# Optimization experiments

Hardware: AMD Instinct MI355X
Metric: run time of the kernel (lower is better)

The kernel has to match this reference:

```python
import jax, jax.numpy as jnp
import numpy as np

D_MODEL = 256
D_ENC_M = 256  # mel encoder dim (keys/values), sets temperature = sqrt(D_ENC_M)
D_ENC_T = 256  # text encoder dim (queries)
LN_EPS = 1e-5


def setup_inputs() -> dict:
    key = jax.random.key(0)
    ks = jax.random.split(key, 9)
    B, MEL_LEN, SRC_LEN = 16, 2048, 512
    mel_encoding = jax.random.normal(ks[0], (B, MEL_LEN, D_ENC_M), dtype=jnp.float32)
    text_encoding = jax.random.normal(ks[1], (B, SRC_LEN, D_ENC_T), dtype=jnp.float32)
    mel_mask = jax.random.randint(ks[2], (B, MEL_LEN), 0, 2).astype(bool)
    src_mask = jax.random.randint(ks[3], (B, SRC_LEN), 0, 2).astype(bool)
    # Linear weights (no bias), xavier-uniform style scale
    def xavier(k, shape):
        fan_in, fan_out = shape[1], shape[0]
        lim = jnp.sqrt(6.0 / (fan_in + fan_out))
        return jax.random.uniform(k, shape, jnp.float32, -lim, lim)
    Wq = xavier(ks[4], (D_MODEL, D_ENC_T))
    Wk = xavier(ks[5], (D_MODEL, D_ENC_M))
    Wv = xavier(ks[6], (D_MODEL, D_ENC_M))
    gamma = jnp.ones((D_MODEL,), jnp.float32)
    beta = jnp.zeros((D_MODEL,), jnp.float32)
    return {"mel_encoding": mel_encoding, "text_encoding": text_encoding,
            "mel_mask": mel_mask, "src_mask": src_mask,
            "Wq": Wq, "Wk": Wk, "Wv": Wv, "gamma": gamma, "beta": beta}


def reference(mel_encoding, text_encoding, mel_mask, src_mask, Wq, Wk, Wv, gamma, beta):
    # QKV projections (nn.Linear, bias=False): y = x @ W^T
    q = jnp.einsum('btd,md->btm', text_encoding, Wq)   # [B, src_len, d_model]
    k = jnp.einsum('bsd,md->bsm', mel_encoding, Wk)    # [B, mel_len, d_model]
    v = jnp.einsum('bsd,md->bsm', mel_encoding, Wv)    # [B, mel_len, d_model]
    temperature = jnp.asarray(D_ENC_M, jnp.float32) ** 0.5
    attn = jnp.einsum('btm,bsm->bts', q, k) / temperature  # [B, src_len, mel_len]
    # pre-softmax fill over mel (key) padding
    attn = jnp.where(mel_mask[:, None, :], -jnp.inf, attn)
    attn = jax.nn.softmax(attn, axis=2)
    # post-softmax zeroing over src (query) padding
    attn = jnp.where(src_mask[:, :, None], 0.0, attn)
    output = jnp.einsum('bts,bsm->btm', attn, v)  # [B, src_len, d_model]
    # dropout is identity in eval mode; LayerNorm over last dim
    mu = jnp.mean(output, axis=-1, keepdims=True)
    var = jnp.mean(jnp.square(output - mu), axis=-1, keepdims=True)
    output = (output - mu) * jax.lax.rsqrt(var + LN_EPS) * gamma + beta
    return (output, attn)
```

## Files before the change

### kernel.cpp

```cpp
#include <hip/hip_runtime.h>
#include <hip/hip_bf16.h>
#include <stdint.h>

#define DMODEL 256
#define BATCH  16
#define MEL    2048
#define SRC    512

typedef __attribute__((ext_vector_type(8))) short bf16x8;
typedef __attribute__((ext_vector_type(4))) short short4v;
typedef __attribute__((ext_vector_type(4))) float f32x4;

__device__ inline short f2bf(float f) {
    union { float f; uint32_t u; } c{f};
    uint32_t u = c.u;
    u += 0x7FFFu + ((u >> 16) & 1u);
    return (short)(u >> 16);
}

__device__ inline bf16x8 cvt8(const float* p) {
    const f32x4* q = reinterpret_cast<const f32x4*>(p);
    f32x4 a = q[0], b = q[1];
    bf16x8 r;
    r[0] = f2bf(a[0]); r[1] = f2bf(a[1]); r[2] = f2bf(a[2]); r[3] = f2bf(a[3]);
    r[4] = f2bf(b[0]); r[5] = f2bf(b[1]); r[6] = f2bf(b[2]); r[7] = f2bf(b[3]);
    return r;
}

__global__ __launch_bounds__(256)
void proj_all_kernel(const float* __restrict__ mel, const float* __restrict__ text,
                     const float* __restrict__ Wq, const float* __restrict__ Wk,
                     const float* __restrict__ Wv,
                     short* __restrict__ qbf, short* __restrict__ kbf,
                     short* __restrict__ vt) {
    __shared__ char SMEM[36864];
    short* As = (short*)SMEM;
    short* Bs = (short*)SMEM + 128 * 72;

    const int tid = threadIdx.x;
    const int lane = tid & 63, w = tid >> 6;
    const int lr = lane & 15, lk = lane >> 4;
    const int wr = w >> 1, wc = w & 1;

    const int u = blockIdx.x;
    const int xcd = u & 7, slot = u >> 3;

    const float *Af, *Bf; short* C; int ldc;
    size_t aro, bro, coff;
    if (slot < 128) {
        const int g = slot >> 2, m = slot & 3;
        const int st = 32 * xcd + g;
        const int b = st >> 4;
        const size_t mr0 = (size_t)(st & 15) * 128;
        if (m < 2) {
            aro = (size_t)b * MEL + mr0;
            bro = (size_t)m * 128;
            Af = mel; Bf = Wk; C = kbf; ldc = DMODEL;
            coff = aro * DMODEL + bro;
        } else {
            aro = (size_t)(m - 2) * 128;
            bro = (size_t)b * MEL + mr0;
            Af = Wv; Bf = mel; C = vt + (size_t)b * DMODEL * MEL; ldc = MEL;
            coff = aro * MEL + mr0;
        }
    } else {
        const int qi = 16 * xcd + (slot - 128);
        aro = (size_t)(qi >> 1) * 128;
        bro = (size_t)(qi & 1) * 128;
        Af = text; Bf = Wq; C = qbf; ldc = DMODEL;
        coff = aro * DMODEL + bro;
    }
    C += coff;

    bf16x8 sA[4], sB[4];
    auto STAGE = [&](int kt) {
#pragma unroll
        for (int i = 0; i < 4; ++i) {
            int idx = i * 256 + tid;
            int row = idx >> 3, c8 = (idx & 7) * 8;
            sA[i] = cvt8(Af + (aro + row) * 256 + kt * 64 + c8);
            sB[i] = cvt8(Bf + (bro + row) * 256 + kt * 64 + c8);
        }
    };

    STAGE(0);
    f32x4 acc[4][4];
#pragma unroll
    for (int m = 0; m < 4; ++m)
#pragma unroll
        for (int n = 0; n < 4; ++n) acc[m][n] = (f32x4){0.f, 0.f, 0.f, 0.f};

    for (int kt = 0; kt < 4; ++kt) {
        __syncthreads();
#pragma unroll
        for (int i = 0; i < 4; ++i) {
            int idx = i * 256 + tid;
            int row = idx >> 3, c8 = (idx & 7) * 8;
            *(bf16x8*)&As[row * 72 + c8] = sA[i];
            *(bf16x8*)&Bs[row * 72 + c8] = sB[i];
        }
        __syncthreads();
        if (kt < 3) STAGE(kt + 1);
#pragma unroll
        for (int kt2 = 0; kt2 < 2; ++kt2) {
            bf16x8 af[4], bfr[4];
#pragma unroll
            for (int m = 0; m < 4; ++m)
                af[m] = *(const bf16x8*)&As[(64 * wr + 16 * m + lr) * 72 + kt2 * 32 + 8 * lk];
#pragma unroll
            for (int n = 0; n < 4; ++n)
                bfr[n] = *(const bf16x8*)&Bs[(64 * wc + 16 * n + lr) * 72 + kt2 * 32 + 8 * lk];
#pragma unroll
            for (int m = 0; m < 4; ++m)
#pragma unroll
                for (int n = 0; n < 4; ++n)
                    acc[m][n] = __builtin_amdgcn_mfma_f32_16x16x32_bf16(af[m], bfr[n], acc[m][n], 0, 0, 0);
        }
    }

    __syncthreads();
    short* Cs = (short*)SMEM;
#pragma unroll
    for (int m = 0; m < 4; ++m)
#pragma unroll
        for (int n = 0; n < 4; ++n)
#pragma unroll
            for (int r = 0; r < 4; ++r)
                Cs[(64 * wr + 16 * m + 4 * lk + r) * 136 + 64 * wc + 16 * n + lr] =
                    f2bf(acc[m][n][r]);
    __syncthreads();
#pragma unroll
    for (int i = 0; i < 8; ++i) {
        int idx = i * 256 + tid;
        int row = idx >> 4, c8 = (idx & 15) * 8;
        *(bf16x8*)&C[(size_t)row * ldc + c8] = *(const bf16x8*)&Cs[row * 136 + c8];
    }
}

__global__ __launch_bounds__(256)
void sgemm_kernel(const short* __restrict__ qbf, const short* __restrict__ kbf,
                  const int* __restrict__ mel_mask,
                  float* __restrict__ attn,
                  float* __restrict__ pmax, float* __restrict__ psum) {
    __shared__ char SMEM[36864];
    short* As = (short*)SMEM;
    short* Bs = (short*)SMEM + 128 * 72;

    const int tid = threadIdx.x;
    const int lane = tid & 63, w = tid >> 6;
    const int lr = lane & 15, lk = lane >> 4;
    const int wr = w >> 1, wc = w & 1;

    const int bid = blockIdx.x;
    const int xcd = bid & 7, j = bid >> 3;
    const int z = 2 * xcd + (j >> 6);
    const int t = j & 63;
    const int x = t & 3, y = t >> 2;

    const short* A = qbf + (size_t)z * SRC * DMODEL + (size_t)x * 128 * DMODEL;
    const short* B = kbf + (size_t)z * MEL * DMODEL + (size_t)y * 128 * DMODEL;
    float* Cw = attn + (size_t)z * SRC * MEL + (size_t)x * 128 * MEL + (size_t)y * 128;

    bf16x8 sA[4], sB[4];
    auto STAGE = [&](int kt) {
#pragma unroll
        for (int i = 0; i < 4; ++i) {
            int idx = i * 256 + tid;
            int row = idx >> 3, c8 = (idx & 7) * 8;
            sA[i] = *(const bf16x8*)(A + (size_t)row * DMODEL + kt * 64 + c8);
            sB[i] = *(const bf16x8*)(B + (size_t)row * DMODEL + kt * 64 + c8);
        }
    };

    STAGE(0);
    f32x4 acc[4][4];
#pragma unroll
    for (int m = 0; m < 4; ++m)
#pragma unroll
        for (int n = 0; n < 4; ++n) acc[m][n] = (f32x4){0.f, 0.f, 0.f, 0.f};

    for (int kt = 0; kt < 4; ++kt) {
        __syncthreads();
#pragma unroll
        for (int i = 0; i < 4; ++i) {
            int idx = i * 256 + tid;
            int row = idx >> 3, c8 = (idx & 7) * 8;
            *(bf16x8*)&As[row * 72 + c8] = sA[i];
            *(bf16x8*)&Bs[row * 72 + c8] = sB[i];
        }
        __syncthreads();
        if (kt < 3) STAGE(kt + 1);
#pragma unroll
        for (int kt2 = 0; kt2 < 2; ++kt2) {
            bf16x8 af[4], bfr[4];
#pragma unroll
            for (int m = 0; m < 4; ++m)
                af[m] = *(const bf16x8*)&As[(64 * wr + 16 * m + lr) * 72 + kt2 * 32 + 8 * lk];
#pragma unroll
            for (int n = 0; n < 4; ++n)
                bfr[n] = *(const bf16x8*)&Bs[(64 * wc + 16 * n + lr) * 72 + kt2 * 32 + 8 * lk];
#pragma unroll
            for (int m = 0; m < 4; ++m)
#pragma unroll
                for (int n = 0; n < 4; ++n)
                    acc[m][n] = __builtin_amdgcn_mfma_f32_16x16x32_bf16(af[m], bfr[n], acc[m][n], 0, 0, 0);
        }
    }

    bool msk[4];
#pragma unroll
    for (int n = 0; n < 4; ++n)
        msk[n] = mel_mask[z * MEL + y * 128 + 64 * wc + 16 * n + lr] != 0;

    __syncthreads();
    float* Cs = (float*)SMEM;
#pragma unroll
    for (int half = 0; half < 2; ++half) {
        if (wr == half) {
#pragma unroll
            for (int m = 0; m < 4; ++m)
#pragma unroll
                for (int n = 0; n < 4; ++n)
#pragma unroll
                    for (int r = 0; r < 4; ++r)
                        Cs[(16 * m + 4 * lk + r) * 132 + 64 * wc + 16 * n + lr] =
                            msk[n] ? -1e30f : acc[m][n][r] * 0.0625f;
        }
        __syncthreads();
#pragma unroll
        for (int i = 0; i < 8; ++i) {
            int idx = i * 256 + tid;
            int row = idx >> 5, c4 = (idx & 31) * 4;
            *(f32x4*)&Cw[(size_t)(half * 64 + row) * MEL + c4] = *(const f32x4*)&Cs[row * 132 + c4];
        }
        {
            const int rrow = tid >> 2, seg = tid & 3;
            const f32x4* crow = (const f32x4*)(Cs + rrow * 132 + seg * 32);
            float m8 = -3.0e38f;
#pragma unroll
            for (int jj = 0; jj < 8; ++jj) {
                f32x4 v = crow[jj];
#pragma unroll
                for (int e = 0; e < 4; ++e) m8 = fmaxf(m8, v[e]);
            }
            m8 = fmaxf(m8, __shfl_xor(m8, 1));
            m8 = fmaxf(m8, __shfl_xor(m8, 2));
            float s8 = 0.f;
#pragma unroll
            for (int jj = 0; jj < 8; ++jj) {
                f32x4 v = crow[jj];
#pragma unroll
                for (int e = 0; e < 4; ++e) s8 += __expf(v[e] - m8);
            }
            s8 += __shfl_xor(s8, 1);
            s8 += __shfl_xor(s8, 2);
            if (seg == 0) {
                int grow = z * SRC + x * 128 + half * 64 + rrow;
                pmax[y * 8192 + grow] = m8;
                psum[y * 8192 + grow] = s8;
            }
        }
        __syncthreads();
    }
}

__global__ __launch_bounds__(512)
void rowred_kernel(const float* __restrict__ pmax, const float* __restrict__ psum,
                   const int* __restrict__ src_mask,
                   float* __restrict__ Mrow, float* __restrict__ Minv) {
    const int row = blockIdx.x * 512 + threadIdx.x;
    float M = -3.0e38f;
#pragma unroll
    for (int i = 0; i < 16; ++i) M = fmaxf(M, pmax[i * 8192 + row]);
    float Z = 0.f;
#pragma unroll
    for (int i = 0; i < 16; ++i)
        Z += psum[i * 8192 + row] * __expf(pmax[i * 8192 + row] - M);
    Mrow[row] = M;
    Minv[row] = (src_mask[row] || !(Z > 0.f)) ? 0.f : 1.f / Z;
}

__global__ __launch_bounds__(512)
void pv_ln_kernel(float* __restrict__ attn, const short* __restrict__ vt,
                  const float* __restrict__ gamma, const float* __restrict__ beta,
                  const float* __restrict__ Mrow, const float* __restrict__ Minv,
                  float* __restrict__ out) {
    __shared__ char SMEM[42496];
    short* As = (short*)SMEM;
    short* Bs = (short*)(SMEM + 4608);
    float* red = (float*)(SMEM + 41472);
    float* Ost = (float*)(SMEM + 4608);

    const int tid = threadIdx.x;
    const int lane = tid & 63, w = tid >> 6;
    const int lr = lane & 15, lk = lane >> 4;
    const int wr = w >> 2, wc = w & 3;

    const int bid = blockIdx.x;
    const int xcd = bid & 7, j = bid >> 3;
    const int b = 2 * xcd + (j >> 4);
    const int mt = j & 15;
    const size_t row0 = (size_t)mt * 32;

    float* A = attn + (size_t)b * SRC * MEL + row0 * MEL;
    const short* Bv = vt + (size_t)b * DMODEL * MEL;

    float gm[4], bt[4];
#pragma unroll
    for (int n = 0; n < 4; ++n) {
        gm[n] = gamma[64 * wc + 16 * n + lr];
        bt[n] = beta[64 * wc + 16 * n + lr];
    }

    const int a_row = tid >> 4, a_c4 = (tid & 15) * 4;
    const float Mr = Mrow[(size_t)b * SRC + row0 + a_row];
    const float Iv = Minv[(size_t)b * SRC + row0 + a_row];

    f32x4 sAv; bf16x8 sB[4];
    auto STAGE = [&](int kt) {
        sAv = *(const f32x4*)(A + (size_t)a_row * MEL + kt * 64 + a_c4);
#pragma unroll
        for (int i = 0; i < 4; ++i) {
            int idx = i * 512 + tid;
            int row = idx >> 3, c8 = (idx & 7) * 8;
            sB[i] = *(const bf16x8*)(Bv + (size_t)row * MEL + kt * 64 + c8);
        }
    };

    STAGE(0);
    f32x4 acc[4];
#pragma unroll
    for (int n = 0; n < 4; ++n) acc[n] = (f32x4){0.f, 0.f, 0.f, 0.f};

    for (int kt = 0; kt < MEL / 64; ++kt) {
        __syncthreads();
        {
            f32x4 p;
#pragma unroll
            for (int e = 0; e < 4; ++e) p[e] = __expf(sAv[e] - Mr) * Iv;
            *(f32x4*)(A + (size_t)a_row * MEL + kt * 64 + a_c4) = p;
            short4v a4 = { f2bf(p[0]), f2bf(p[1]), f2bf(p[2]), f2bf(p[3]) };
            *(short4v*)&As[a_row * 72 + a_c4] = a4;
#pragma unroll
            for (int i = 0; i < 4; ++i) {
                int idx = i * 512 + tid;
                int row = idx >> 3, c8 = (idx & 7) * 8;
                *(bf16x8*)&Bs[row * 72 + c8] = sB[i];
            }
        }
        __syncthreads();
        if (kt + 1 < MEL / 64) STAGE(kt + 1);
#pragma unroll
        for (int kt2 = 0; kt2 < 2; ++kt2) {
            bf16x8 af = *(const bf16x8*)&As[(16 * wr + lr) * 72 + kt2 * 32 + 8 * lk];
#pragma unroll
            for (int n = 0; n < 4; ++n) {
                bf16x8 bfr = *(const bf16x8*)&Bs[(64 * wc + 16 * n + lr) * 72 + kt2 * 32 + 8 * lk];
                acc[n] = __builtin_amdgcn_mfma_f32_16x16x32_bf16(af, bfr, acc[n], 0, 0, 0);
            }
        }
    }

    float s1[4] = {0.f, 0.f, 0.f, 0.f}, s2[4] = {0.f, 0.f, 0.f, 0.f};
#pragma unroll
    for (int n = 0; n < 4; ++n)
#pragma unroll
        for (int r = 0; r < 4; ++r) {
            s1[r] += acc[n][r];
            s2[r] += acc[n][r] * acc[n][r];
        }
#pragma unroll
    for (int off = 8; off; off >>= 1)
#pragma unroll
        for (int r = 0; r < 4; ++r) {
            s1[r] += __shfl_xor(s1[r], off);
            s2[r] += __shfl_xor(s2[r], off);
        }
    __syncthreads();
    if (lr == 0) {
#pragma unroll
        for (int r = 0; r < 4; ++r) {
            red[(16 * wr + 4 * lk + r) * 4 + wc] = s1[r];
            red[128 + (16 * wr + 4 * lk + r) * 4 + wc] = s2[r];
        }
    }
    __syncthreads();
    float mu[4], rsig[4];
#pragma unroll
    for (int r = 0; r < 4; ++r) {
        int rowi = 16 * wr + 4 * lk + r;
        float S1 = red[rowi * 4 + 0] + red[rowi * 4 + 1] + red[rowi * 4 + 2] + red[rowi * 4 + 3];
        float S2 = red[128 + rowi * 4 + 0] + red[128 + rowi * 4 + 1] +
                   red[128 + rowi * 4 + 2] + red[128 + rowi * 4 + 3];
        mu[r] = S1 * (1.f / DMODEL);
        rsig[r] = rsqrtf(S2 * (1.f / DMODEL) - mu[r] * mu[r] + 1e-5f);
    }
    __syncthreads();
#pragma unroll
    for (int n = 0; n < 4; ++n)
#pragma unroll
        for (int r = 0; r < 4; ++r)
            Ost[(16 * wr + 4 * lk + r) * 260 + 64 * wc + 16 * n + lr] =
                (acc[n][r] - mu[r]) * rsig[r] * gm[n] + bt[n];
    __syncthreads();
#pragma unroll
    for (int i = 0; i < 4; ++i) {
        int idx = i * 512 + tid;
        int row = idx >> 6, c4 = (idx & 63) * 4;
        *(f32x4*)&out[((size_t)b * SRC + row0 + row) * DMODEL + c4] =
            *(const f32x4*)&Ost[row * 260 + c4];
    }
}

extern "C" void kernel_launch(void* const* d_in, const int* in_sizes, int n_in,
                              void* d_out, int out_size, void* d_ws, size_t ws_size,
                              hipStream_t stream) {
    const float* mel      = (const float*)d_in[0];
    const float* text     = (const float*)d_in[1];
    const int*   mel_mask = (const int*)d_in[2];
    const int*   src_mask = (const int*)d_in[3];
    const float* Wq       = (const float*)d_in[4];
    const float* Wk       = (const float*)d_in[5];
    const float* Wv       = (const float*)d_in[6];
    const float* gamma    = (const float*)d_in[7];
    const float* beta     = (const float*)d_in[8];

    float* out  = (float*)d_out;
    float* attn = out + (size_t)BATCH * SRC * DMODEL;

    short* qbf = (short*)d_ws;
    short* kbf = qbf + (size_t)BATCH * SRC * DMODEL;
    short* vt  = kbf + (size_t)BATCH * MEL * DMODEL;
    float* pmax = (float*)(vt + (size_t)BATCH * DMODEL * MEL);
    float* psum = pmax + 16 * 8192;
    float* Mrow = psum + 16 * 8192;
    float* Minv = Mrow + 8192;

    proj_all_kernel<<<1152, 256, 0, stream>>>(mel, text, Wq, Wk, Wv, qbf, kbf, vt);
    sgemm_kernel<<<1024, 256, 0, stream>>>(qbf, kbf, mel_mask, attn, pmax, psum);
    rowred_kernel<<<16, 512, 0, stream>>>(pmax, psum, src_mask, Mrow, Minv);
    pv_ln_kernel<<<256, 512, 0, stream>>>(attn, vt, gamma, beta, Mrow, Minv, out);
}
```

Before: 202.9 us.

## Halve GEMM tile widths to double block counts across all three kernels

Shrinks the N dimension of the projection and score GEMM tiles from 128 to 64, and the PV+LayerNorm row tile from 32 to 16 rows, doubling grid sizes and adding occupancy hints via launch_bounds. The goal is to fill the 256 CUs more evenly and raise occupancy through smaller LDS and register footprints. In exchange each block reuses less data, the A operand is reloaded more often, and there are twice as many partial max/sum entries to reduce. In pv_ln, half the threads now sit idle during the A staging.

```diff
diff --git a/kernel.cpp b/kernel.cpp
--- a/kernel.cpp
+++ b/kernel.cpp
@@ -27,13 +27,13 @@
     return r;
 }
 
-__global__ __launch_bounds__(256)
+__global__ __launch_bounds__(256, 4)
 void proj_all_kernel(const float* __restrict__ mel, const float* __restrict__ text,
                      const float* __restrict__ Wq, const float* __restrict__ Wk,
                      const float* __restrict__ Wv,
                      short* __restrict__ qbf, short* __restrict__ kbf,
                      short* __restrict__ vt) {
-    __shared__ char SMEM[36864];
+    __shared__ char SMEM[27648];
     short* As = (short*)SMEM;
     short* Bs = (short*)SMEM + 128 * 72;
 
@@ -43,77 +43,86 @@
     const int wr = w >> 1, wc = w & 1;
 
     const int u = blockIdx.x;
-    const int xcd = u & 7, slot = u >> 3;
-
     const float *Af, *Bf; short* C; int ldc;
-    size_t aro, bro, coff;
-    if (slot < 128) {
-        const int g = slot >> 2, m = slot & 3;
-        const int st = 32 * xcd + g;
-        const int b = st >> 4;
-        const size_t mr0 = (size_t)(st & 15) * 128;
-        if (m < 2) {
+    size_t aro, bro;
+    if (u < 2048) {
+        const int xcd = u & 7, t = u >> 3;
+        const int kind = t & 7, sg = t >> 3;
+        const int stripe = (sg << 3) | xcd;
+        const int b = stripe >> 4;
+        const size_t mr0 = (size_t)(stripe & 15) * 128;
+        if (kind < 4) {
             aro = (size_t)b * MEL + mr0;
-            bro = (size_t)m * 128;
-            Af = mel; Bf = Wk; C = kbf; ldc = DMODEL;
-            coff = aro * DMODEL + bro;
+            bro = (size_t)kind * 64;
+            Af = mel; Bf = Wk; ldc = DMODEL;
+            C = kbf + aro * DMODEL + bro;
         } else {
-            aro = (size_t)(m - 2) * 128;
-            bro = (size_t)b * MEL + mr0;
-            Af = Wv; Bf = mel; C = vt + (size_t)b * DMODEL * MEL; ldc = MEL;
-            coff = aro * MEL + mr0;
+            const int kk = kind - 4;
+            aro = (size_t)(kk >> 1) * 128;
+            bro = (size_t)b * MEL + mr0 + (size_t)(kk & 1) * 64;
+            Af = Wv; Bf = mel; ldc = MEL;
+            C = vt + (size_t)b * DMODEL * MEL + aro * MEL + mr0 + (size_t)(kk & 1) * 64;
         }
     } else {
-        const int qi = 16 * xcd + (slot - 128);
-        aro = (size_t)(qi >> 1) * 128;
-        bro = (size_t)(qi & 1) * 128;
-        Af = text; Bf = Wq; C = qbf; ldc = DMODEL;
-        coff = aro * DMODEL + bro;
-    }
-    C += coff;
-
-    bf16x8 sA[4], sB[4];
+        const int v = u - 2048;
+        const int xcd = v & 7, qj = v >> 3;
+        const int mt = 8 * xcd + (qj >> 2), nt = qj & 3;
+        aro = (size_t)mt * 128;
+        bro = (size_t)nt * 64;
+        Af = text; Bf = Wq; ldc = DMODEL;
+        C = qbf + aro * DMODEL + bro;
+    }
+
+    bf16x8 sA[4], sB[2];
     auto STAGE = [&](int kt) {
 #pragma unroll
         for (int i = 0; i < 4; ++i) {
             int idx = i * 256 + tid;
             int row = idx >> 3, c8 = (idx & 7) * 8;
             sA[i] = cvt8(Af + (aro + row) * 256 + kt * 64 + c8);
+        }
+#pragma unroll
+        for (int i = 0; i < 2; ++i) {
+            int idx = i * 256 + tid;
+            int row = idx >> 3, c8 = (idx & 7) * 8;
             sB[i] = cvt8(Bf + (bro + row) * 256 + kt * 64 + c8);
         }
     };
 
     STAGE(0);
-    f32x4 acc[4][4];
+    f32x4 acc[4][2];
 #pragma unroll
     for (int m = 0; m < 4; ++m)
 #pragma unroll
-        for (int n = 0; n < 4; ++n) acc[m][n] = (f32x4){0.f, 0.f, 0.f, 0.f};
+        for (int n = 0; n < 2; ++n) acc[m][n] = (f32x4){0.f, 0.f, 0.f, 0.f};
 
     for (int kt = 0; kt < 4; ++kt) {
         __syncthreads();
 #pragma unroll
         for (int i = 0; i < 4; ++i) {
             int idx = i * 256 + tid;
-            int row = idx >> 3, c8 = (idx & 7) * 8;
-            *(bf16x8*)&As[row * 72 + c8] = sA[i];
-            *(bf16x8*)&Bs[row * 72 + c8] = sB[i];
+            *(bf16x8*)&As[(idx >> 3) * 72 + (idx & 7) * 8] = sA[i];
+        }
+#pragma unroll
+        for (int i = 0; i < 2; ++i) {
+            int idx = i * 256 + tid;
+            *(bf16x8*)&Bs[(idx >> 3) * 72 + (idx & 7) * 8] = sB[i];
         }
         __syncthreads();
         if (kt < 3) STAGE(kt + 1);
 #pragma unroll
         for (int kt2 = 0; kt2 < 2; ++kt2) {
-            bf16x8 af[4], bfr[4];
+            bf16x8 af[4], bfr[2];
 #pragma unroll
             for (int m = 0; m < 4; ++m)
                 af[m] = *(const bf16x8*)&As[(64 * wr + 16 * m + lr) * 72 + kt2 * 32 + 8 * lk];
 #pragma unroll
-            for (int n = 0; n < 4; ++n)
-                bfr[n] = *(const bf16x8*)&Bs[(64 * wc + 16 * n + lr) * 72 + kt2 * 32 + 8 * lk];
+            for (int n = 0; n < 2; ++n)
+                bfr[n] = *(const bf16x8*)&Bs[(32 * wc + 16 * n + lr) * 72 + kt2 * 32 + 8 * lk];
 #pragma unroll
             for (int m = 0; m < 4; ++m)
 #pragma unroll
-                for (int n = 0; n < 4; ++n)
+                for (int n = 0; n < 2; ++n)
                     acc[m][n] = __builtin_amdgcn_mfma_f32_16x16x32_bf16(af[m], bfr[n], acc[m][n], 0, 0, 0);
         }
     }
@@ -123,26 +132,26 @@
 #pragma unroll
     for (int m = 0; m < 4; ++m)
 #pragma unroll
-        for (int n = 0; n < 4; ++n)
+        for (int n = 0; n < 2; ++n)
 #pragma unroll
             for (int r = 0; r < 4; ++r)
-                Cs[(64 * wr + 16 * m + 4 * lk + r) * 136 + 64 * wc + 16 * n + lr] =
+                Cs[(64 * wr + 16 * m + 4 * lk + r) * 72 + 32 * wc + 16 * n + lr] =
                     f2bf(acc[m][n][r]);
     __syncthreads();
 #pragma unroll
-    for (int i = 0; i < 8; ++i) {
+    for (int i = 0; i < 4; ++i) {
         int idx = i * 256 + tid;
-        int row = idx >> 4, c8 = (idx & 15) * 8;
-        *(bf16x8*)&C[(size_t)row * ldc + c8] = *(const bf16x8*)&Cs[row * 136 + c8];
-    }
-}
-
-__global__ __launch_bounds__(256)
+        int row = idx >> 3, c8 = (idx & 7) * 8;
+        *(bf16x8*)&C[(size_t)row * ldc + c8] = *(const bf16x8*)&Cs[row * 72 + c8];
+    }
+}
+
+__global__ __launch_bounds__(256, 4)
 void sgemm_kernel(const short* __restrict__ qbf, const short* __restrict__ kbf,
                   const int* __restrict__ mel_mask,
                   float* __restrict__ attn,
                   float* __restrict__ pmax, float* __restrict__ psum) {
-    __shared__ char SMEM[36864];
+    __shared__ char SMEM[27648];
     short* As = (short*)SMEM;
     short* Bs = (short*)SMEM + 128 * 72;
 
@@ -153,64 +162,70 @@
 
     const int bid = blockIdx.x;
     const int xcd = bid & 7, j = bid >> 3;
-    const int z = 2 * xcd + (j >> 6);
-    const int t = j & 63;
+    const int z = 2 * xcd + (j >> 7);
+    const int t = j & 127;
     const int x = t & 3, y = t >> 2;
 
     const short* A = qbf + (size_t)z * SRC * DMODEL + (size_t)x * 128 * DMODEL;
-    const short* B = kbf + (size_t)z * MEL * DMODEL + (size_t)y * 128 * DMODEL;
-    float* Cw = attn + (size_t)z * SRC * MEL + (size_t)x * 128 * MEL + (size_t)y * 128;
-
-    bf16x8 sA[4], sB[4];
+    const short* B = kbf + (size_t)z * MEL * DMODEL + (size_t)y * 64 * DMODEL;
+    float* Cw = attn + (size_t)z * SRC * MEL + (size_t)x * 128 * MEL + (size_t)y * 64;
+
+    bf16x8 sA[4], sB[2];
     auto STAGE = [&](int kt) {
 #pragma unroll
         for (int i = 0; i < 4; ++i) {
             int idx = i * 256 + tid;
-            int row = idx >> 3, c8 = (idx & 7) * 8;
-            sA[i] = *(const bf16x8*)(A + (size_t)row * DMODEL + kt * 64 + c8);
-            sB[i] = *(const bf16x8*)(B + (size_t)row * DMODEL + kt * 64 + c8);
+            sA[i] = *(const bf16x8*)(A + (size_t)(idx >> 3) * DMODEL + kt * 64 + (idx & 7) * 8);
+        }
+#pragma unroll
+        for (int i = 0; i < 2; ++i) {
+            int idx = i * 256 + tid;
+            sB[i] = *(const bf16x8*)(B + (size_t)(idx >> 3) * DMODEL + kt * 64 + (idx & 7) * 8);
         }
     };
 
     STAGE(0);
-    f32x4 acc[4][4];
+    f32x4 acc[4][2];
 #pragma unroll
     for (int m = 0; m < 4; ++m)
 #pragma unroll
-        for (int n = 0; n < 4; ++n) acc[m][n] = (f32x4){0.f, 0.f, 0.f, 0.f};
+        for (int n = 0; n < 2; ++n) acc[m][n] = (f32x4){0.f, 0.f, 0.f, 0.f};
 
     for (int kt = 0; kt < 4; ++kt) {
         __syncthreads();
 #pragma unroll
         for (int i = 0; i < 4; ++i) {
             int idx = i * 256 + tid;
-            int row = idx >> 3, c8 = (idx & 7) * 8;
-            *(bf16x8*)&As[row * 72 + c8] = sA[i];
-            *(bf16x8*)&Bs[row * 72 + c8] = sB[i];
+            *(bf16x8*)&As[(idx >> 3) * 72 + (idx & 7) * 8] = sA[i];
+        }
+#pragma unroll
+        for (int i = 0; i < 2; ++i) {
+            int idx = i * 256 + tid;
+            *(bf16x8*)&Bs[(idx >> 3) * 72 + (idx & 7) * 8] = sB[i];
         }
         __syncthreads();
         if (kt < 3) STAGE(kt + 1);
 #pragma unroll
         for (int kt2 = 0; kt2 < 2; ++kt2) {
-            bf16x8 af[4], bfr[4];
+            bf16x8 af[4], bfr[2];
 #pragma unroll
             for (int m = 0; m < 4; ++m)
                 af[m] = *(const bf16x8*)&As[(64 * wr + 16 * m + lr) * 72 + kt2 * 32 + 8 * lk];
 #pragma unroll
-            for (int n = 0; n < 4; ++n)
-                bfr[n] = *(const bf16x8*)&Bs[(64 * wc + 16 * n + lr) * 72 + kt2 * 32 + 8 * lk];
+            for (int n = 0; n < 2; ++n)
+                bfr[n] = *(const bf16x8*)&Bs[(32 * wc + 16 * n + lr) * 72 + kt2 * 32 + 8 * lk];
 #pragma unroll
             for (int m = 0; m < 4; ++m)
 #pragma unroll
-                for (int n = 0; n < 4; ++n)
+                for (int n = 0; n < 2; ++n)
                     acc[m][n] = __builtin_amdgcn_mfma_f32_16x16x32_bf16(af[m], bfr[n], acc[m][n], 0, 0, 0);
         }
     }
 
-    bool msk[4];
-#pragma unroll
-    for (int n = 0; n < 4; ++n)
-        msk[n] = mel_mask[z * MEL + y * 128 + 64 * wc + 16 * n + lr] != 0;
+    bool msk[2];
+#pragma unroll
+    for (int n = 0; n < 2; ++n)
+        msk[n] = mel_mask[z * MEL + y * 64 + 32 * wc + 16 * n + lr] != 0;
 
     __syncthreads();
     float* Cs = (float*)SMEM;
@@ -220,37 +235,37 @@
 #pragma unroll
             for (int m = 0; m < 4; ++m)
 #pragma unroll
-                for (int n = 0; n < 4; ++n)
+                for (int n = 0; n < 2; ++n)
 #pragma unroll
                     for (int r = 0; r < 4; ++r)
-                        Cs[(16 * m + 4 * lk + r) * 132 + 64 * wc + 16 * n + lr] =
+                        Cs[(16 * m + 4 * lk + r) * 68 + 32 * wc + 16 * n + lr] =
                             msk[n] ? -1e30f : acc[m][n][r] * 0.0625f;
         }
         __syncthreads();
 #pragma unroll
-        for (int i = 0; i < 8; ++i) {
-            int idx = i * 256 + tid;
-            int row = idx >> 5, c4 = (idx & 31) * 4;
-            *(f32x4*)&Cw[(size_t)(half * 64 + row) * MEL + c4] = *(const f32x4*)&Cs[row * 132 + c4];
+        for (int i = 0; i < 4; ++i) {
+            int idx = i * 256 + tid;
+            int row = idx >> 4, c4 = (idx & 15) * 4;
+            *(f32x4*)&Cw[(size_t)(half * 64 + row) * MEL + c4] = *(const f32x4*)&Cs[row * 68 + c4];
         }
         {
             const int rrow = tid >> 2, seg = tid & 3;
-            const f32x4* crow = (const f32x4*)(Cs + rrow * 132 + seg * 32);
+            const f32x4* crow = (const f32x4*)(Cs + rrow * 68 + seg * 16);
             float m8 = -3.0e38f;
 #pragma unroll
-            for (int jj = 0; jj < 8; ++jj) {
-                f32x4 v = crow[jj];
-#pragma unroll
-                for (int e = 0; e < 4; ++e) m8 = fmaxf(m8, v[e]);
+            for (int jj = 0; jj < 4; ++jj) {
+                f32x4 vv = crow[jj];
+#pragma unroll
+                for (int e = 0; e < 4; ++e) m8 = fmaxf(m8, vv[e]);
             }
             m8 = fmaxf(m8, __shfl_xor(m8, 1));
             m8 = fmaxf(m8, __shfl_xor(m8, 2));
             float s8 = 0.f;
 #pragma unroll
-            for (int jj = 0; jj < 8; ++jj) {
-                f32x4 v = crow[jj];
-#pragma unroll
-                for (int e = 0; e < 4; ++e) s8 += __expf(v[e] - m8);
+            for (int jj = 0; jj < 4; ++jj) {
+                f32x4 vv = crow[jj];
+#pragma unroll
+                for (int e = 0; e < 4; ++e) s8 += __expf(vv[e] - m8);
             }
             s8 += __shfl_xor(s8, 1);
             s8 += __shfl_xor(s8, 2);
@@ -271,91 +286,92 @@
     const int row = blockIdx.x * 512 + threadIdx.x;
     float M = -3.0e38f;
 #pragma unroll
-    for (int i = 0; i < 16; ++i) M = fmaxf(M, pmax[i * 8192 + row]);
+    for (int i = 0; i < 32; ++i) M = fmaxf(M, pmax[i * 8192 + row]);
     float Z = 0.f;
 #pragma unroll
-    for (int i = 0; i < 16; ++i)
+    for (int i = 0; i < 32; ++i)
         Z += psum[i * 8192 + row] * __expf(pmax[i * 8192 + row] - M);
     Mrow[row] = M;
     Minv[row] = (src_mask[row] || !(Z > 0.f)) ? 0.f : 1.f / Z;
 }
 
-__global__ __launch_bounds__(512)
+__global__ __launch_bounds__(512, 4)
 void pv_ln_kernel(float* __restrict__ attn, const short* __restrict__ vt,
                   const float* __restrict__ gamma, const float* __restrict__ beta,
                   const float* __restrict__ Mrow, const float* __restrict__ Minv,
                   float* __restrict__ out) {
-    __shared__ char SMEM[42496];
+    __shared__ char SMEM[39168];
     short* As = (short*)SMEM;
-    short* Bs = (short*)(SMEM + 4608);
-    float* red = (float*)(SMEM + 41472);
-    float* Ost = (float*)(SMEM + 4608);
+    short* Bs = (short*)(SMEM + 2304);
+    float* red = (float*)SMEM;
+    float* Ost = (float*)(SMEM + 2304);
 
     const int tid = threadIdx.x;
     const int lane = tid & 63, w = tid >> 6;
     const int lr = lane & 15, lk = lane >> 4;
-    const int wr = w >> 2, wc = w & 3;
 
     const int bid = blockIdx.x;
     const int xcd = bid & 7, j = bid >> 3;
-    const int b = 2 * xcd + (j >> 4);
-    const int mt = j & 15;
-    const size_t row0 = (size_t)mt * 32;
+    const int b = 2 * xcd + (j >> 5);
+    const int mt = j & 31;
+    const size_t row0 = (size_t)mt * 16;
 
     float* A = attn + (size_t)b * SRC * MEL + row0 * MEL;
     const short* Bv = vt + (size_t)b * DMODEL * MEL;
 
-    float gm[4], bt[4];
-#pragma unroll
-    for (int n = 0; n < 4; ++n) {
-        gm[n] = gamma[64 * wc + 16 * n + lr];
-        bt[n] = beta[64 * wc + 16 * n + lr];
-    }
-
-    const int a_row = tid >> 4, a_c4 = (tid & 15) * 4;
-    const float Mr = Mrow[(size_t)b * SRC + row0 + a_row];
-    const float Iv = Minv[(size_t)b * SRC + row0 + a_row];
+    float gm[2], bt[2];
+#pragma unroll
+    for (int n = 0; n < 2; ++n) {
+        gm[n] = gamma[32 * w + 16 * n + lr];
+        bt[n] = beta[32 * w + 16 * n + lr];
+    }
+
+    const int a_row = (tid & 255) >> 4, a_c4 = (tid & 15) * 4;
+    float Mr = 0.f, Iv = 0.f;
+    if (tid < 256) {
+        Mr = Mrow[(size_t)b * SRC + row0 + a_row];
+        Iv = Minv[(size_t)b * SRC + row0 + a_row];
+    }
 
     f32x4 sAv; bf16x8 sB[4];
     auto STAGE = [&](int kt) {
-        sAv = *(const f32x4*)(A + (size_t)a_row * MEL + kt * 64 + a_c4);
+        if (tid < 256)
+            sAv = *(const f32x4*)(A + (size_t)a_row * MEL + kt * 64 + a_c4);
 #pragma unroll
         for (int i = 0; i < 4; ++i) {
             int idx = i * 512 + tid;
-            int row = idx >> 3, c8 = (idx & 7) * 8;
-            sB[i] = *(const bf16x8*)(Bv + (size_t)row * MEL + kt * 64 + c8);
+            sB[i] = *(const bf16x8*)(Bv + (size_t)(idx >> 3) * MEL + kt * 64 + (idx & 7) * 8);
         }
     };
 
     STAGE(0);
-    f32x4 acc[4];
-#pragma unroll
-    for (int n = 0; n < 4; ++n) acc[n] = (f32x4){0.f, 0.f, 0.f, 0.f};
+    f32x4 acc[2];
+    acc[0] = (f32x4){0.f, 0.f, 0.f, 0.f};
+    acc[1] = (f32x4){0.f, 0.f, 0.f, 0.f};
 
     for (int kt = 0; kt < MEL / 64; ++kt) {
         __syncthreads();
-        {
+        if (tid < 256) {
             f32x4 p;
 #pragma unroll
             for (int e = 0; e < 4; ++e) p[e] = __expf(sAv[e] - Mr) * Iv;
             *(f32x4*)(A + (size_t)a_row * MEL + kt * 64 + a_c4) = p;
             short4v a4 = { f2bf(p[0]), f2bf(p[1]), f2bf(p[2]), f2bf(p[3]) };
             *(short4v*)&As[a_row * 72 + a_c4] = a4;
-#pragma unroll
-            for (int i = 0; i < 4; ++i) {
-                int idx = i * 512 + tid;
-                int row = idx >> 3, c8 = (idx & 7) * 8;
-                *(bf16x8*)&Bs[row * 72 + c8] = sB[i];
-            }
+        }
+#pragma unroll
+        for (int i = 0; i < 4; ++i) {
+            int idx = i * 512 + tid;
+            *(bf16x8*)&Bs[(idx >> 3) * 72 + (idx & 7) * 8] = sB[i];
         }
         __syncthreads();
         if (kt + 1 < MEL / 64) STAGE(kt + 1);
 #pragma unroll
         for (int kt2 = 0; kt2 < 2; ++kt2) {
-            bf16x8 af = *(const bf16x8*)&As[(16 * wr + lr) * 72 + kt2 * 32 + 8 * lk];
-#pragma unroll
-            for (int n = 0; n < 4; ++n) {
-                bf16x8 bfr = *(const bf16x8*)&Bs[(64 * wc + 16 * n + lr) * 72 + kt2 * 32 + 8 * lk];
+            bf16x8 af = *(const bf16x8*)&As[lr * 72 + kt2 * 32 + 8 * lk];
+#pragma unroll
+            for (int n = 0; n < 2; ++n) {
+                bf16x8 bfr = *(const bf16x8*)&Bs[(32 * w + 16 * n + lr) * 72 + kt2 * 32 + 8 * lk];
                 acc[n] = __builtin_amdgcn_mfma_f32_16x16x32_bf16(af, bfr, acc[n], 0, 0, 0);
             }
         }
@@ -363,7 +379,7 @@
 
     float s1[4] = {0.f, 0.f, 0.f, 0.f}, s2[4] = {0.f, 0.f, 0.f, 0.f};
 #pragma unroll
-    for (int n = 0; n < 4; ++n)
+    for (int n = 0; n < 2; ++n)
 #pragma unroll
         for (int r = 0; r < 4; ++r) {
             s1[r] += acc[n][r];
@@ -380,31 +396,34 @@
     if (lr == 0) {
 #pragma unroll
         for (int r = 0; r < 4; ++r) {
-            red[(16 * wr + 4 * lk + r) * 4 + wc] = s1[r];
-            red[128 + (16 * wr + 4 * lk + r) * 4 + wc] = s2[r];
+            red[(4 * lk + r) * 8 + w] = s1[r];
+            red[128 + (4 * lk + r) * 8 + w] = s2[r];
         }
     }
     __syncthreads();
     float mu[4], rsig[4];
 #pragma unroll
     for (int r = 0; r < 4; ++r) {
-        int rowi = 16 * wr + 4 * lk + r;
-        float S1 = red[rowi * 4 + 0] + red[rowi * 4 + 1] + red[rowi * 4 + 2] + red[rowi * 4 + 3];
-        float S2 = red[128 + rowi * 4 + 0] + red[128 + rowi * 4 + 1] +
-                   red[128 + rowi * 4 + 2] + red[128 + rowi * 4 + 3];
+        const int rowi = 4 * lk + r;
+        float S1 = 0.f, S2 = 0.f;
+#pragma unroll
+        for (int ww = 0; ww < 8; ++ww) {
+            S1 += red[rowi * 8 + ww];
+            S2 += red[128 + rowi * 8 + ww];
+        }
         mu[r] = S1 * (1.f / DMODEL);
         rsig[r] = rsqrtf(S2 * (1.f / DMODEL) - mu[r] * mu[r] + 1e-5f);
     }
     __syncthreads();
 #pragma unroll
-    for (int n = 0; n < 4; ++n)
+    for (int n = 0; n < 2; ++n)
 #pragma unroll
         for (int r = 0; r < 4; ++r)
-            Ost[(16 * wr + 4 * lk + r) * 260 + 64 * wc + 16 * n + lr] =
+            Ost[(4 * lk + r) * 260 + 32 * w + 16 * n + lr] =
                 (acc[n][r] - mu[r]) * rsig[r] * gm[n] + bt[n];
     __syncthreads();
 #pragma unroll
-    for (int i = 0; i < 4; ++i) {
+    for (int i = 0; i < 2; ++i) {
         int idx = i * 512 + tid;
         int row = idx >> 6, c4 = (idx & 63) * 4;
         *(f32x4*)&out[((size_t)b * SRC + row0 + row) * DMODEL + c4] =
@@ -432,12 +451,12 @@
     short* kbf = qbf + (size_t)BATCH * SRC * DMODEL;
     short* vt  = kbf + (size_t)BATCH * MEL * DMODEL;
     float* pmax = (float*)(vt + (size_t)BATCH * DMODEL * MEL);
-    float* psum = pmax + 16 * 8192;
-    float* Mrow = psum + 16 * 8192;
+    float* psum = pmax + 32 * 8192;
+    float* Mrow = psum + 32 * 8192;
     float* Minv = Mrow + 8192;
 
-    proj_all_kernel<<<1152, 256, 0, stream>>>(mel, text, Wq, Wk, Wv, qbf, kbf, vt);
-    sgemm_kernel<<<1024, 256, 0, stream>>>(qbf, kbf, mel_mask, attn, pmax, psum);
+    proj_all_kernel<<<2304, 256, 0, stream>>>(mel, text, Wq, Wk, Wv, qbf, kbf, vt);
+    sgemm_kernel<<<2048, 256, 0, stream>>>(qbf, kbf, mel_mask, attn, pmax, psum);
     rowred_kernel<<<16, 512, 0, stream>>>(pmax, psum, src_mask, Mrow, Minv);
-    pv_ln_kernel<<<256, 512, 0, stream>>>(attn, vt, gamma, beta, Mrow, Minv, out);
-}
+    pv_ln_kernel<<<512, 512, 0, stream>>>(attn, vt, gamma, beta, Mrow, Minv, out);
+}
```

Result: slower. 212.6 us (+4.8%).
